# Kernel tuning notes

Measured on AMD Instinct MI355X. Metric: run time of the kernel, lower is better.

The kernel has to match this reference:

```python
import jax, jax.numpy as jnp
import numpy as np

EMBED_DIM = 64
NUM_CODES = 4096
BETA = 0.25  # commitment_cost


def setup_inputs() -> dict:
    key = jax.random.key(0)
    k1, k2 = jax.random.split(key)
    inputs = jax.random.normal(k1, (512, 8192, 1), dtype=jnp.float32)
    # tf.random_uniform_initializer default range [0, 0.05)
    embeddings = jax.random.uniform(k2, (EMBED_DIM, NUM_CODES), dtype=jnp.float32, minval=0.0, maxval=0.05)
    return {"inputs": inputs, "embeddings": embeddings}


def reference(inputs, embeddings):
    # MuModel.call, training=False (no EMA state updates at inference)
    x = inputs[:, :, 0]                       # [B, T]
    flat = x.reshape(-1, EMBED_DIM)           # [N, D]
    # squared L2 distances to each code: ||z||^2 - 2 z.E + ||e||^2  -> [N, K]
    distances = (
        jnp.sum(flat * flat, axis=1, keepdims=True)
        - 2.0 * (flat @ embeddings)
        + jnp.sum(embeddings * embeddings, axis=0, keepdims=True)
    )
    # tf uses argmax(-distances) == argmin(distances)
    idx = jnp.argmax(-distances, axis=1)      # [N] int
    # one-hot @ embeddings.T is just a gather of code vectors
    quantized = jnp.take(embeddings.T, idx, axis=0)   # [N, D]
    quantized = quantized.reshape(x.shape)            # [B, T]
    commitment_loss = BETA * jnp.mean((jax.lax.stop_gradient(quantized) - x) ** 2)
    quantized = x + jax.lax.stop_gradient(quantized - x)  # straight-through
    out = quantized[..., None]                # [B, T, 1]
    return (out, commitment_loss, idx)
```

## Files before the change

kernel.cpp:

```cpp
#include <hip/hip_runtime.h>
#include <float.h>

#define EMBED   64
#define CODES   4096
#define NROWS   65536
#define NELEM   4194304
#define BR      128
#define NTILE   128
#define TUNITS  512

typedef __attribute__((ext_vector_type(8)))  short bf16x8;
typedef __attribute__((ext_vector_type(16))) float f32x16;

__device__ inline unsigned short f2bf(float f) {
    unsigned u = __float_as_uint(f);
    u += 0x7fff + ((u >> 16) & 1);
    return (unsigned short)(u >> 16);
}
__device__ inline float bf2f(unsigned short h) {
    return __uint_as_float(((unsigned)h) << 16);
}

__global__ void vq_setup(const float* __restrict__ E, float* __restrict__ cbuf,
                         double* __restrict__ accum, bf16x8* __restrict__ packed,
                         float* __restrict__ ET) {
    const int b = blockIdx.x, t = threadIdx.x;
    if (b < 16) {
        int j = b * 256 + t;
        float v = E[j];
        float s = __fmul_rn(v, v);
        for (int i = 1; i < EMBED; ++i) {
            v = E[(size_t)i * CODES + j];
            s = __fadd_rn(s, __fmul_rn(v, v));
        }
        cbuf[j] = s;
        if (j == 0) *accum = 0.0;
    } else if (b < 144) {
        int id = (b - 16) * 256 + t;
        int lam = id & 63, kk = (id >> 6) & 3, g = id >> 8;
        int n  = g * 32 + (lam & 31);
        int kb = kk * 16 + (lam >> 5) * 8;
        bf16x8 vh, vl;
#pragma unroll
        for (int j = 0; j < 8; ++j) {
            float e = E[(size_t)(kb + j) * CODES + n];
            unsigned short hi = f2bf(e);
            vh[j] = (short)hi;
            vl[j] = (short)f2bf(e - bf2f(hi));
        }
        packed[((g * 4 + kk) * 2 + 0) * 64 + lam] = vh;
        packed[((g * 4 + kk) * 2 + 1) * 64 + lam] = vl;
    } else {
        int id = (b - 144) * 256 + t;
        int j = id >> 4, i0 = (id & 15) * 4;
        float4 v;
        v.x = E[(size_t)(i0 + 0) * CODES + j];
        v.y = E[(size_t)(i0 + 1) * CODES + j];
        v.z = E[(size_t)(i0 + 2) * CODES + j];
        v.w = E[(size_t)(i0 + 3) * CODES + j];
        *(float4*)(ET + (size_t)j * EMBED + i0) = v;
    }
}

template <bool PRE>
__global__ __launch_bounds__(256, 2)
void vq_main(const float* __restrict__ X, const float* __restrict__ E,
             const float* __restrict__ cbuf, const bf16x8* __restrict__ packed,
             const float* __restrict__ ET, double* __restrict__ accum,
             float* __restrict__ out) {
    __shared__ float rowm1[BR], rowsq[BR];
    __shared__ int   rowidx[BR], rowflg[BR];
    __shared__ float fredv[256];
    __shared__ int   fredi[256];

    const int t  = threadIdx.x;
    const int l  = t & 63, wv = t >> 6;
    const int m  = l & 31, h  = l >> 5;
    const int row0 = blockIdx.x * BR;

    bf16x8 ah[4], al[4];
    float sqreg;
    {
        const float* xrow = X + (size_t)(row0 + wv * 32 + m) * EMBED;
        float sq = 0.f;
#pragma unroll
        for (int kk = 0; kk < 4; ++kk) {
            int kb = kk * 16 + h * 8;
            float4 v0 = *(const float4*)(xrow + kb);
            float4 v1 = *(const float4*)(xrow + kb + 4);
            float xv[8] = {v0.x, v0.y, v0.z, v0.w, v1.x, v1.y, v1.z, v1.w};
#pragma unroll
            for (int j = 0; j < 8; ++j) {
                sq = fmaf(xv[j], xv[j], sq);
                unsigned short hi = f2bf(xv[j]);
                float r = xv[j] - bf2f(hi);
                ah[kk][j] = (short)hi;
                al[kk][j] = (short)f2bf(r);
            }
        }
        sq += __shfl_xor(sq, 32, 64);
        sqreg = sq;
    }

    float M1[16], M2[16];
#pragma unroll
    for (int e = 0; e < 16; ++e) { M1[e] = -FLT_MAX; M2[e] = -FLT_MAX; }

    auto process = [&](const bf16x8 (&B)[8], float nc, int g) {
        f32x16 acc;
#pragma unroll
        for (int e = 0; e < 16; ++e) acc[e] = nc;
#pragma unroll
        for (int kk = 0; kk < 4; ++kk) {
            acc = __builtin_amdgcn_mfma_f32_32x32x16_bf16(ah[kk], B[kk * 2],     acc, 0, 0, 0);
            acc = __builtin_amdgcn_mfma_f32_32x32x16_bf16(ah[kk], B[kk * 2 + 1], acc, 0, 0, 0);
            acc = __builtin_amdgcn_mfma_f32_32x32x16_bf16(al[kk], B[kk * 2],     acc, 0, 0, 0);
        }
        unsigned gu = (unsigned)g;
#pragma unroll
        for (int e = 0; e < 16; ++e) {
            float ap = __uint_as_float((__float_as_uint(acc[e]) & 0xFFFFFF80u) | gu);
            float m1o = M1[e];
            M1[e] = fmaxf(m1o, ap);
            M2[e] = __builtin_amdgcn_fmed3f(m1o, M2[e], ap);
        }
    };

    if constexpr (PRE) {
        bf16x8 Ba[8], Bb[8];
        float ncA, ncB;
        {
            const bf16x8* p = packed + l;
#pragma unroll
            for (int q = 0; q < 8; ++q) Ba[q] = p[q * 64];
            ncA = -0.5f * cbuf[m];
        }
#pragma unroll 1
        for (int g = 0; g < NTILE; g += 2) {
            {
                const bf16x8* p = packed + (size_t)(g + 1) * TUNITS + l;
#pragma unroll
                for (int q = 0; q < 8; ++q) Bb[q] = p[q * 64];
                ncB = -0.5f * cbuf[(g + 1) * 32 + m];
            }
            process(Ba, ncA, g);
            if (g + 2 < NTILE) {
                const bf16x8* p = packed + (size_t)(g + 2) * TUNITS + l;
#pragma unroll
                for (int q = 0; q < 8; ++q) Ba[q] = p[q * 64];
                ncA = -0.5f * cbuf[(g + 2) * 32 + m];
            }
            process(Bb, ncB, g + 1);
        }
    } else {
#pragma unroll 1
        for (int g = 0; g < NTILE; ++g) {
            bf16x8 B[8];
            int n = g * 32 + m;
#pragma unroll
            for (int kk = 0; kk < 4; ++kk) {
                const float* ec = E + (size_t)(kk * 16 + h * 8) * CODES + n;
                bf16x8 vh, vl;
#pragma unroll
                for (int j = 0; j < 8; ++j) {
                    float e = ec[(size_t)j * CODES];
                    unsigned short hi = f2bf(e);
                    vh[j] = (short)hi;
                    vl[j] = (short)f2bf(e - bf2f(hi));
                }
                B[kk * 2] = vh; B[kk * 2 + 1] = vl;
            }
            process(B, -0.5f * cbuf[g * 32 + m], g);
        }
    }

    int I1[16];
#pragma unroll
    for (int e = 0; e < 16; ++e)
        I1[e] = (int)(((__float_as_uint(M1[e]) & 0x7Fu) << 5) | (unsigned)m);
#pragma unroll
    for (int d = 1; d < 32; d <<= 1) {
#pragma unroll
        for (int e = 0; e < 16; ++e) {
            float oM1 = __shfl_xor(M1[e], d, 64);
            float oM2 = __shfl_xor(M2[e], d, 64);
            int   oI  = __shfl_xor(I1[e], d, 64);
            float lo  = fminf(M1[e], oM1);
            M2[e] = fmaxf(lo, fmaxf(M2[e], oM2));
            bool c = oM1 > M1[e];
            I1[e] = c ? oI : I1[e];
            M1[e] = c ? oM1 : M1[e];
        }
    }
    if (h == 0) rowsq[wv * 32 + m] = sqreg;
#pragma unroll
    for (int e = 0; e < 16; ++e) {
        int r = (e & 3) + 8 * (e >> 2) + 4 * h;
        if (m == r) {
            rowm1[wv * 32 + r]  = __uint_as_float(__float_as_uint(M1[e]) & 0xFFFFFF80u);
            rowidx[wv * 32 + r] = I1[e];
            rowflg[wv * 32 + r] = (2.f * (M1[e] - M2[e]) < 2e-4f) ? 1 : 0;
        }
    }
    __syncthreads();

#pragma unroll 1
    for (int r = 0; r < BR; ++r) {
        if (rowflg[r] == 0) continue;
        const float* xr = X + (size_t)(row0 + r) * EMBED;
        float racc[8];
#pragma unroll
        for (int jq = 0; jq < 8; ++jq) racc[jq] = __fmul_rn(xr[jq], xr[jq]);
#pragma unroll
        for (int i = 8; i < 64; i += 8)
#pragma unroll
            for (int jq = 0; jq < 8; ++jq)
                racc[jq] = __fadd_rn(racc[jq], __fmul_rn(xr[i + jq], xr[i + jq]));
        float A = __fadd_rn(
            __fadd_rn(__fadd_rn(racc[0], racc[1]), __fadd_rn(racc[2], racc[3])),
            __fadd_rn(__fadd_rn(racc[4], racc[5]), __fadd_rn(racc[6], racc[7])));

        float best = FLT_MAX; int bestj = CODES;
#pragma unroll 1
        for (int jj = 0; jj < 16; ++jj) {
            int j = jj * 256 + t;
            float mm = 0.f;
#pragma unroll
            for (int i = 0; i < 64; ++i)
                mm = fmaf(xr[i], E[(size_t)i * CODES + j], mm);
            float d = __fadd_rn(__fsub_rn(A, __fmul_rn(2.f, mm)), cbuf[j]);
            if (d < best || (d == best && j < bestj)) { best = d; bestj = j; }
        }
        fredv[t] = best; fredi[t] = bestj;
        __syncthreads();
        if (t == 0) {
            float B = fredv[0]; int BI = fredi[0];
            for (int c2 = 1; c2 < 256; ++c2) {
                float dc = fredv[c2]; int jc = fredi[c2];
                if (dc < B || (dc == B && jc < BI)) { B = dc; BI = jc; }
            }
            rowidx[r] = BI;
        }
        __syncthreads();
    }

    if (t < BR) out[(size_t)NELEM + 1 + row0 + t] = (float)rowidx[t];
    if (t == 0) {
        float bs = 0.f;
        for (int r = 0; r < BR; ++r) bs += rowsq[r] - 2.f * rowm1[r];
        atomicAdd(accum, (double)bs);
    }
    {
        int r = t >> 1, i0 = (t & 1) * 32;
        int j = rowidx[r];
        float* dst = out + (size_t)(row0 + r) * EMBED + i0;
        if constexpr (PRE) {
            const float* src = ET + (size_t)j * EMBED + i0;
#pragma unroll
            for (int g = 0; g < 8; ++g)
                *(float4*)(dst + g * 4) = *(const float4*)(src + g * 4);
        } else {
#pragma unroll
            for (int g = 0; g < 8; ++g) {
                float4 v;
                v.x = E[(size_t)(i0 + g * 4 + 0) * CODES + j];
                v.y = E[(size_t)(i0 + g * 4 + 1) * CODES + j];
                v.z = E[(size_t)(i0 + g * 4 + 2) * CODES + j];
                v.w = E[(size_t)(i0 + g * 4 + 3) * CODES + j];
                *(float4*)(dst + g * 4) = v;
            }
        }
    }
}

__global__ void vq_finalize(const double* __restrict__ accum, float* __restrict__ out) {
    out[NELEM] = (float)(0.25 * (*accum) / (double)NELEM);
}

extern "C" void kernel_launch(void* const* d_in, const int* in_sizes, int n_in,
                              void* d_out, int out_size, void* d_ws, size_t ws_size,
                              hipStream_t stream) {
    const float* X = (const float*)d_in[0];
    const float* E = (const float*)d_in[1];
    float* out = (float*)d_out;
    float*  cbuf   = (float*)d_ws;
    double* accum  = (double*)((char*)d_ws + 16384);
    bf16x8* packed = (bf16x8*)((char*)d_ws + 32768);
    float*  ET     = (float*)((char*)d_ws + 32768 + 1048576);
    const size_t need = 32768 + 1048576 + 1048576;
    const bool pre = (ws_size >= need);

    vq_setup<<<pre ? 400 : 16, 256, 0, stream>>>(E, cbuf, accum, packed, ET);
    if (pre)
        vq_main<true><<<NROWS / BR, 256, 0, stream>>>(X, E, cbuf, packed, ET, accum, out);
    else
        vq_main<false><<<NROWS / BR, 256, 0, stream>>>(X, E, cbuf, packed, ET, accum, out);
    vq_finalize<<<1, 1, 0, stream>>>(accum, out);
}
```

Before: 291.3 us.

## Stage codebook chunks into LDS via async global_load_lds with double buffering

```diff
diff --git a/kernel.cpp b/kernel.cpp
--- a/kernel.cpp
+++ b/kernel.cpp
@@ -6,8 +6,10 @@
 #define NROWS   65536
 #define NELEM   4194304
 #define BR      128
+#define CCH     128
+#define NCH     32
+#define CUNITS  2048
 #define NTILE   128
-#define TUNITS  512
 
 typedef __attribute__((ext_vector_type(8)))  short bf16x8;
 typedef __attribute__((ext_vector_type(16))) float f32x16;
@@ -68,10 +70,7 @@
              const float* __restrict__ cbuf, const bf16x8* __restrict__ packed,
              const float* __restrict__ ET, double* __restrict__ accum,
              float* __restrict__ out) {
-    __shared__ float rowm1[BR], rowsq[BR];
-    __shared__ int   rowidx[BR], rowflg[BR];
-    __shared__ float fredv[256];
-    __shared__ int   fredi[256];
+    __shared__ bf16x8 lbuf[2][CUNITS];
 
     const int t  = threadIdx.x;
     const int l  = t & 63, wv = t >> 6;
@@ -106,20 +105,11 @@
 #pragma unroll
     for (int e = 0; e < 16; ++e) { M1[e] = -FLT_MAX; M2[e] = -FLT_MAX; }
 
-    auto process = [&](const bf16x8 (&B)[8], float nc, int g) {
-        f32x16 acc;
-#pragma unroll
-        for (int e = 0; e < 16; ++e) acc[e] = nc;
-#pragma unroll
-        for (int kk = 0; kk < 4; ++kk) {
-            acc = __builtin_amdgcn_mfma_f32_32x32x16_bf16(ah[kk], B[kk * 2],     acc, 0, 0, 0);
-            acc = __builtin_amdgcn_mfma_f32_32x32x16_bf16(ah[kk], B[kk * 2 + 1], acc, 0, 0, 0);
-            acc = __builtin_amdgcn_mfma_f32_32x32x16_bf16(al[kk], B[kk * 2],     acc, 0, 0, 0);
-        }
+    auto epi = [&](const f32x16& a, int g) {
         unsigned gu = (unsigned)g;
 #pragma unroll
         for (int e = 0; e < 16; ++e) {
-            float ap = __uint_as_float((__float_as_uint(acc[e]) & 0xFFFFFF80u) | gu);
+            float ap = __uint_as_float((__float_as_uint(a[e]) & 0xFFFFFF80u) | gu);
             float m1o = M1[e];
             M1[e] = fmaxf(m1o, ap);
             M2[e] = __builtin_amdgcn_fmed3f(m1o, M2[e], ap);
@@ -127,31 +117,66 @@
     };
 
     if constexpr (PRE) {
-        bf16x8 Ba[8], Bb[8];
-        float ncA, ncB;
-        {
-            const bf16x8* p = packed + l;
-#pragma unroll
-            for (int q = 0; q < 8; ++q) Ba[q] = p[q * 64];
-            ncA = -0.5f * cbuf[m];
-        }
+        auto stage = [&](int ch, int buf) {
+#pragma unroll
+            for (int q = 0; q < 8; ++q) {
+                const bf16x8* gp = packed + (size_t)ch * CUNITS + q * 256 + t;
+                bf16x8* lp = &lbuf[buf][q * 256 + wv * 64];
+                __builtin_amdgcn_global_load_lds(
+                    (const __attribute__((address_space(1))) void*)gp,
+                    (__attribute__((address_space(3))) void*)lp, 16, 0, 0);
+            }
+        };
+
+        f32x16 pA, pB; int pGA = 0, pGB = 0;
+#pragma unroll
+        for (int e = 0; e < 16; ++e) { pA[e] = -FLT_MAX; pB[e] = -FLT_MAX; }
+
+        const int ch0 = blockIdx.x & (NCH - 1);
+        stage(ch0, 0);
+        __syncthreads();
+
+        int b = 0;
 #pragma unroll 1
-        for (int g = 0; g < NTILE; g += 2) {
-            {
-                const bf16x8* p = packed + (size_t)(g + 1) * TUNITS + l;
-#pragma unroll
-                for (int q = 0; q < 8; ++q) Bb[q] = p[q * 64];
-                ncB = -0.5f * cbuf[(g + 1) * 32 + m];
-            }
-            process(Ba, ncA, g);
-            if (g + 2 < NTILE) {
-                const bf16x8* p = packed + (size_t)(g + 2) * TUNITS + l;
-#pragma unroll
-                for (int q = 0; q < 8; ++q) Ba[q] = p[q * 64];
-                ncA = -0.5f * cbuf[(g + 2) * 32 + m];
-            }
-            process(Bb, ncB, g + 1);
-        }
+        for (int cc = 0; cc < NCH; ++cc) {
+            int ch = ch0 + cc; if (ch >= NCH) ch -= NCH;
+            if (cc + 1 < NCH) { int cn = ch + 1; if (cn >= NCH) cn -= NCH; stage(cn, b ^ 1); }
+            const bf16x8* lb = lbuf[b];
+#pragma unroll
+            for (int pp = 0; pp < 2; ++pp) {
+                const int tl0 = pp * 2, tl1 = tl0 + 1;
+                const int g0 = ch * 4 + tl0, g1 = ch * 4 + tl1;
+                bf16x8 B0[8], B1[8];
+#pragma unroll
+                for (int kk = 0; kk < 4; ++kk) {
+                    B0[kk * 2]     = lb[tl0 * 512 + kk * 128 + l];
+                    B0[kk * 2 + 1] = lb[tl0 * 512 + kk * 128 + 64 + l];
+                    B1[kk * 2]     = lb[tl1 * 512 + kk * 128 + l];
+                    B1[kk * 2 + 1] = lb[tl1 * 512 + kk * 128 + 64 + l];
+                }
+                float nc0 = -0.5f * cbuf[g0 * 32 + m];
+                float nc1 = -0.5f * cbuf[g1 * 32 + m];
+                epi(pA, pGA);
+                epi(pB, pGB);
+                f32x16 a0, a1;
+#pragma unroll
+                for (int e = 0; e < 16; ++e) { a0[e] = nc0; a1[e] = nc1; }
+#pragma unroll
+                for (int kk = 0; kk < 4; ++kk) {
+                    a0 = __builtin_amdgcn_mfma_f32_32x32x16_bf16(ah[kk], B0[kk * 2],     a0, 0, 0, 0);
+                    a1 = __builtin_amdgcn_mfma_f32_32x32x16_bf16(ah[kk], B1[kk * 2],     a1, 0, 0, 0);
+                    a0 = __builtin_amdgcn_mfma_f32_32x32x16_bf16(ah[kk], B0[kk * 2 + 1], a0, 0, 0, 0);
+                    a1 = __builtin_amdgcn_mfma_f32_32x32x16_bf16(ah[kk], B1[kk * 2 + 1], a1, 0, 0, 0);
+                    a0 = __builtin_amdgcn_mfma_f32_32x32x16_bf16(al[kk], B0[kk * 2],     a0, 0, 0, 0);
+                    a1 = __builtin_amdgcn_mfma_f32_32x32x16_bf16(al[kk], B1[kk * 2],     a1, 0, 0, 0);
+                }
+                pA = a0; pB = a1; pGA = g0; pGB = g1;
+            }
+            __syncthreads();
+            b ^= 1;
+        }
+        epi(pA, pGA);
+        epi(pB, pGB);
     } else {
 #pragma unroll 1
         for (int g = 0; g < NTILE; ++g) {
@@ -170,9 +195,27 @@
                 }
                 B[kk * 2] = vh; B[kk * 2 + 1] = vl;
             }
-            process(B, -0.5f * cbuf[g * 32 + m], g);
-        }
-    }
+            float nc = -0.5f * cbuf[g * 32 + m];
+            f32x16 acc;
+#pragma unroll
+            for (int e = 0; e < 16; ++e) acc[e] = nc;
+#pragma unroll
+            for (int kk = 0; kk < 4; ++kk) {
+                acc = __builtin_amdgcn_mfma_f32_32x32x16_bf16(ah[kk], B[kk * 2],     acc, 0, 0, 0);
+                acc = __builtin_amdgcn_mfma_f32_32x32x16_bf16(ah[kk], B[kk * 2 + 1], acc, 0, 0, 0);
+                acc = __builtin_amdgcn_mfma_f32_32x32x16_bf16(al[kk], B[kk * 2],     acc, 0, 0, 0);
+            }
+            epi(acc, g);
+        }
+        __syncthreads();
+    }
+
+    float* rowm1  = (float*)&lbuf[0][0];
+    float* rowsq  = rowm1 + BR;
+    int*   rowidx = (int*)(rowsq + BR);
+    int*   rowflg = rowidx + BR;
+    float* fredv  = (float*)(rowflg + BR);
+    int*   fredi  = (int*)(fredv + 256);
 
     int I1[16];
 #pragma unroll
```

Measured after the change: 262.0 us. -10.1%, faster.
